# Kernel tuning notes

Measured on AMD Instinct MI355X. Metric: run time of the kernel, lower is better.

## Reference

```python
import jax, jax.numpy as jnp
import numpy as np

LN_EPS = 1e-5

def _layernorm(x, g, b):
    m = jnp.mean(x, axis=-1, keepdims=True)
    v = jnp.var(x, axis=-1, keepdims=True)
    return (x - m) * jax.lax.rsqrt(v + LN_EPS) * g + b

def setup_inputs() -> dict:
    key = jax.random.key(0)
    ks = jax.random.split(key, 8)
    H = 1024
    B, S = 8, 2048
    def xavier(k, fan_in, fan_out):
        lim = float(np.sqrt(6.0 / (fan_in + fan_out)))
        return jax.random.uniform(k, (fan_in, fan_out), jnp.float32, -lim, lim)
    return {
        "x": jax.random.normal(ks[0], (B, S, H), jnp.float32),
        "hidden_state": jnp.zeros((B, H), jnp.float32),
        "W_in": xavier(ks[1], H, 3 * H), "b_in": jnp.zeros((3 * H,), jnp.float32),
        "W_rec": xavier(ks[2], H, H), "b_rec": jnp.zeros((H,), jnp.float32),
        "W_gate": xavier(ks[3], H, 2 * H), "b_gate": jnp.zeros((2 * H,), jnp.float32),
        "W_out": xavier(ks[4], H, H), "b_out": jnp.zeros((H,), jnp.float32),
        "ln_g": jnp.ones((H,), jnp.float32), "ln_b": jnp.zeros((H,), jnp.float32),
    }

def reference(x, hidden_state, W_in, b_in, W_rec, b_rec, W_gate, b_gate, W_out, b_out, ln_g, ln_b):
    # x: [B, S, H]
    H = x.shape[-1]
    feats = jnp.einsum('bsh,hk->bsk', x, W_in) + b_in        # [B,S,3H]
    u, v, w = jnp.split(feats, 3, axis=-1)
    u = jax.nn.silu(u)
    v = jax.nn.silu(v)
    # scan over time: xs laid out [S, B, H]
    uvw = (u.swapaxes(0, 1), v.swapaxes(0, 1), w.swapaxes(0, 1))

    def step(h, xs_t):
        u_t, v_t, w_t = xs_t
        gf = h @ W_gate + b_gate                              # [B,2H]
        gv, gt = jnp.split(gf, 2, axis=-1)
        gate = jax.nn.sigmoid(gv) * jax.nn.silu(gt)
        rec = h @ W_rec + b_rec
        nh = gate * rec + (1.0 - gate) * (u_t * v_t + w_t)
        nh = _layernorm(nh, ln_g, ln_b)                       # dropout inactive (eval)
        return nh, nh

    final_hidden, hiddens = jax.lax.scan(step, hidden_state, uvw)  # hiddens: [S,B,H]
    output = jnp.einsum('sbh,hk->bsk', hiddens, W_out) + b_out     # [B,S,H]
    return output, final_hidden
```

## Files before the change

### kernel.cpp

```cpp
#include <hip/hip_runtime.h>
#include <stdint.h>
#include <stddef.h>

typedef _Float16 f16;
typedef __attribute__((ext_vector_type(8))) _Float16 f16x8;
typedef __attribute__((ext_vector_type(4))) _Float16 f16x4;
typedef __attribute__((ext_vector_type(4))) float     f32x4;
typedef unsigned long long u64;

#define NB 8
#define NS 2048
#define NHID 1024
#define NWG 64

__device__ __forceinline__ float fsig(float x)  { return 1.f/(1.f+__expf(-x)); }
__device__ __forceinline__ float fsilu(float x) { return x/(1.f+__expf(-x)); }

__global__ __launch_bounds__(256) void k_cvt_f16(const float* __restrict__ in,
                                                 f16* __restrict__ out, int n) {
  int i = (blockIdx.x*blockDim.x + threadIdx.x)*4;
  int stride = gridDim.x*blockDim.x*4;
  for (; i < n; i += stride) {
    f32x4 v = *(const f32x4*)(in + i);
    f16x4 o = { (f16)v[0], (f16)v[1], (f16)v[2], (f16)v[3] };
    *(f16x4*)(out + i) = o;
  }
}

__global__ __launch_bounds__(256) void k_transpose_cvt(const float* __restrict__ W,
                                                       f16* __restrict__ Wt,
                                                       int K, int N) {
  __shared__ float tile[32][33];
  int k0 = blockIdx.x*32, n0 = blockIdx.y*32;
  int tx = threadIdx.x & 31, ty = threadIdx.x >> 5;
  for (int i = ty; i < 32; i += 8) tile[i][tx] = W[(size_t)(k0+i)*N + n0 + tx];
  __syncthreads();
  for (int i = ty; i < 32; i += 8) Wt[(size_t)(n0+i)*K + k0 + tx] = (f16)tile[tx][i];
}

__global__ __launch_bounds__(256) void k_gemm1(const f16* __restrict__ A,
                                               const f16* __restrict__ Bt,
                                               const float* __restrict__ b_in,
                                               f16* __restrict__ z) {
  __shared__ f16 As[2][128*64];
  __shared__ f16 Bs[2][3][32*64];
  const int tid  = threadIdx.x;
  const int row0 = blockIdx.x * 128;
  const int j0   = blockIdx.y * 32;
  const int lane = tid & 63, wave = tid >> 6;
  const int wm = wave >> 1, wj = wave & 1;

  f32x4 acc[4][3];
  const f32x4 zv = {0.f,0.f,0.f,0.f};
#pragma unroll
  for (int m = 0; m < 4; ++m)
#pragma unroll
    for (int s = 0; s < 3; ++s) acc[m][s] = zv;

  f16x8 ar[4]; f16x8 br[3];

  auto loadT = [&](int kt) {
    int k0 = kt*64;
#pragma unroll
    for (int i = 0; i < 4; ++i) {
      int c = tid + i*256; int r = c >> 3;
      ar[i] = *(const f16x8*)(A + (size_t)(row0 + r)*1024 + k0 + (c & 7)*8);
    }
#pragma unroll
    for (int i = 0; i < 3; ++i) {
      int c = tid + i*256; int strip = c >> 8; int cc = c & 255; int r = cc >> 3;
      br[i] = *(const f16x8*)(Bt + (size_t)(strip*1024 + j0 + r)*1024 + k0 + (cc & 7)*8);
    }
  };
  auto writeT = [&](int buf) {
#pragma unroll
    for (int i = 0; i < 4; ++i) {
      int c = tid + i*256; int r = c >> 3; int kb = (c & 7)*16;
      *(f16x8*)((char*)As[buf] + r*128 + (kb ^ ((r & 7) << 4))) = ar[i];
    }
#pragma unroll
    for (int i = 0; i < 3; ++i) {
      int c = tid + i*256; int strip = c >> 8; int cc = c & 255; int r = cc >> 3; int kb = (cc & 7)*16;
      *(f16x8*)((char*)Bs[buf][strip] + r*128 + (kb ^ ((r & 7) << 4))) = br[i];
    }
  };
  auto compute = [&](int buf) {
    const char* Ab = (const char*)As[buf];
#pragma unroll
    for (int kk = 0; kk < 2; ++kk) {
      int kq = kk*64 + ((lane >> 4) << 4);
      f16x8 af[4];
#pragma unroll
      for (int mt = 0; mt < 4; ++mt) {
        int r = wm*64 + mt*16 + (lane & 15);
        af[mt] = *(const f16x8*)(Ab + r*128 + (kq ^ ((r & 7) << 4)));
      }
#pragma unroll
      for (int st = 0; st < 3; ++st) {
        int cB = wj*16 + (lane & 15);
        f16x8 bf = *(const f16x8*)((const char*)Bs[buf][st] + cB*128 + (kq ^ ((cB & 7) << 4)));
#pragma unroll
        for (int mt = 0; mt < 4; ++mt)
          acc[mt][st] = __builtin_amdgcn_mfma_f32_16x16x32_f16(af[mt], bf, acc[mt][st], 0, 0, 0);
      }
    }
  };

  loadT(0); writeT(0);
  __syncthreads();
  for (int kt = 0; kt < 16; ++kt) {
    int cur = kt & 1;
    if (kt + 1 < 16) loadT(kt+1);
    compute(cur);
    if (kt + 1 < 16) writeT(cur ^ 1);
    __syncthreads();
  }

  const int jc = j0 + wj*16 + (lane & 15);
  const float bu = b_in[jc], bv = b_in[1024 + jc], bw = b_in[2048 + jc];
#pragma unroll
  for (int mt = 0; mt < 4; ++mt) {
#pragma unroll
    for (int i = 0; i < 4; ++i) {
      int r = row0 + wm*64 + mt*16 + ((lane >> 4) << 2) + i;
      float u = acc[mt][0][i] + bu;
      float v = acc[mt][1][i] + bv;
      float w = acc[mt][2][i] + bw;
      float zz = fsilu(u)*fsilu(v) + w;
      int b_ = r >> 11, s_ = r & 2047;
      z[(((size_t)s_*64 + (jc >> 4))*8 + b_)*16 + (jc & 15)] = (f16)zz;
    }
  }
}

__global__ __launch_bounds__(256) void k_gemm3(const f16* __restrict__ A,
                                               const f16* __restrict__ Bt,
                                               const float* __restrict__ b_out,
                                               float* __restrict__ out) {
  __shared__ f16 As[2][128*64];
  __shared__ f16 Bs[2][32*64];
  const int tid  = threadIdx.x;
  const int row0 = blockIdx.x * 128;
  const int n0   = blockIdx.y * 32;
  const int lane = tid & 63, wave = tid >> 6;
  const int wm = wave >> 1, wn = wave & 1;

  f32x4 acc[4];
  const f32x4 zv = {0.f,0.f,0.f,0.f};
#pragma unroll
  for (int m = 0; m < 4; ++m) acc[m] = zv;

  f16x8 ar[4]; f16x8 br1;

  auto loadT = [&](int kt) {
    int k0 = kt*64;
#pragma unroll
    for (int i = 0; i < 4; ++i) {
      int c = tid + i*256; int r = c >> 3;
      ar[i] = *(const f16x8*)(A + (size_t)(row0 + r)*1024 + k0 + (c & 7)*8);
    }
    { int c = tid; int r = c >> 3;
      br1 = *(const f16x8*)(Bt + (size_t)(n0 + r)*1024 + k0 + (c & 7)*8); }
  };
  auto writeT = [&](int buf) {
#pragma unroll
    for (int i = 0; i < 4; ++i) {
      int c = tid + i*256; int r = c >> 3; int kb = (c & 7)*16;
      *(f16x8*)((char*)As[buf] + r*128 + (kb ^ ((r & 7) << 4))) = ar[i];
    }
    { int c = tid; int r = c >> 3; int kb = (c & 7)*16;
      *(f16x8*)((char*)Bs[buf] + r*128 + (kb ^ ((r & 7) << 4))) = br1; }
  };
  auto compute = [&](int buf) {
    const char* Ab = (const char*)As[buf];
#pragma unroll
    for (int kk = 0; kk < 2; ++kk) {
      int kq = kk*64 + ((lane >> 4) << 4);
      int cB = wn*16 + (lane & 15);
      f16x8 bf = *(const f16x8*)((const char*)Bs[buf] + cB*128 + (kq ^ ((cB & 7) << 4)));
#pragma unroll
      for (int mt = 0; mt < 4; ++mt) {
        int r = wm*64 + mt*16 + (lane & 15);
        f16x8 af = *(const f16x8*)(Ab + r*128 + (kq ^ ((r & 7) << 4)));
        acc[mt] = __builtin_amdgcn_mfma_f32_16x16x32_f16(af, bf, acc[mt], 0, 0, 0);
      }
    }
  };

  loadT(0); writeT(0);
  __syncthreads();
  for (int kt = 0; kt < 16; ++kt) {
    int cur = kt & 1;
    if (kt + 1 < 16) loadT(kt+1);
    compute(cur);
    if (kt + 1 < 16) writeT(cur ^ 1);
    __syncthreads();
  }

  const int n = n0 + wn*16 + (lane & 15);
  const float bo = b_out[n];
#pragma unroll
  for (int mt = 0; mt < 4; ++mt) {
#pragma unroll
    for (int i = 0; i < 4; ++i) {
      int r = row0 + wm*64 + mt*16 + ((lane >> 4) << 2) + i;
      int s = r >> 3, b = r & 7;
      out[(size_t)b*(NS*NHID) + (size_t)s*NHID + n] = acc[mt][i] + bo;
    }
  }
}

#define SCAN_LDS 70848
__global__ __launch_bounds__(256, 1) void k_scan(
    const float* __restrict__ h0g,  const float* __restrict__ Wg,
    const float* __restrict__ bg,   const float* __restrict__ Wr,
    const float* __restrict__ brv,  const float* __restrict__ lng_g,
    const float* __restrict__ lnb_g,const f16* __restrict__ z,
    f16* __restrict__ hid,          u64* __restrict__ hpub,
    float* __restrict__ finalh) {
  extern __shared__ char smem[];
  f16*   hlds = (f16*)smem;
  f16*   nhst = (f16*)(smem + 33536);
  float* red  = (float*)(smem + 49920);
  float* lng  = (float*)(smem + 62208);
  float* lnb  = (float*)(smem + 66304);
  float* bia  = (float*)(smem + 70400);
  f16*   pub  = (f16*)(smem + 70592);

  const int tid  = threadIdx.x;
  const int wg   = blockIdx.x;
  const int wave = tid >> 6, lane = tid & 63;
  const int r8   = tid >> 5, g32 = tid & 31;
  const int rr   = (tid >> 4) & 7, cc = tid & 15;

  f16x8 wf0[8], wf1[8], wf2[8];
  {
    const int cB = wg*16 + (lane & 15);
    const int kq = (lane >> 4) << 3;
#pragma unroll
    for (int ks = 0; ks < 8; ++ks) {
      int k = wave*256 + ks*32 + kq;
      f16x8 a, b, c;
#pragma unroll
      for (int e = 0; e < 8; ++e) {
        a[e] = (f16)Wg[(size_t)(k+e)*2048 + cB];
        b[e] = (f16)Wg[(size_t)(k+e)*2048 + 1024 + cB];
        c[e] = (f16)Wr[(size_t)(k+e)*1024 + cB];
      }
      wf0[ks] = a; wf1[ks] = b; wf2[ks] = c;
    }
  }
  for (int i = tid; i < 1024; i += 256) { lng[i] = lng_g[i]; lnb[i] = lnb_g[i]; }
  if (tid < 48)
    bia[tid] = (tid < 16) ? bg[wg*16 + tid]
             : (tid < 32) ? bg[1024 + wg*16 + (tid-16)]
                          : brv[wg*16 + (tid-32)];
  for (int i = tid; i < 8*1048; i += 256) hlds[8*1048 + i] = (f16)0.f;
  __syncthreads();

  for (int t = 0; t <= NS; ++t) {
    f16 zreg = (f16)0.f;
    if (t < NS && tid < 128) zreg = z[(((size_t)t*64 + wg)*8 + rr)*16 + cc];

    if (t == 0) {
#pragma unroll
      for (int j = 0; j < 8; ++j) {
        f32x4 v = *(const f32x4*)(h0g + r8*1024 + (j*32 + g32)*4);
        int colb = j*128 + g32*4;
        f16x4 hv = { (f16)v[0], (f16)v[1], (f16)v[2], (f16)v[3] };
        *(f16x4*)(hlds + r8*1048 + colb) = hv;
      }
      __syncthreads();
    } else {
      const u64* src = hpub + (size_t)(t & 1)*2816;
      u64 got[11];
      unsigned ok = 0;
      while (!ok) {
        ok = 1;
#pragma unroll
        for (int i = 0; i < 11; ++i) {
          got[i] = __hip_atomic_load(src + i*256 + tid,
                                     __ATOMIC_RELAXED, __HIP_MEMORY_SCOPE_AGENT);
          ok &= (unsigned)((unsigned)(got[i] >> 48) == (unsigned)t);
        }
      }
#pragma unroll
      for (int i = 0; i < 11; ++i) {
        int gidx = i*256 + tid;
        int wgI = gidx / 44;
        int slot = gidx - wgI*44;
        if (slot < 43) {
          int s0 = slot*3;
          u64 g = got[i];
#pragma unroll
          for (int e = 0; e < 3; ++e) {
            int s = s0 + e;
            if (s < 128) {
              unsigned short hb = (unsigned short)(g >> (16*e));
              nhst[((s >> 4))*1024 + wgI*16 + (s & 15)] = __builtin_bit_cast(f16, hb);
            }
          }
        }
      }
      __syncthreads();

      float sum = 0.f, sq = 0.f;
#pragma unroll
      for (int j = 0; j < 8; ++j) {
        f16x4 hv = *(const f16x4*)(nhst + r8*1024 + (j*32 + g32)*4);
#pragma unroll
        for (int e = 0; e < 4; ++e) { float v = (float)hv[e]; sum += v; sq += v*v; }
      }
#pragma unroll
      for (int off = 16; off > 0; off >>= 1) {
        sum += __shfl_xor(sum, off, 32);
        sq  += __shfl_xor(sq,  off, 32);
      }
      float m  = sum * (1.f/1024.f);
      float va = sq  * (1.f/1024.f) - m*m;
      float rs = rsqrtf(va + 1e-5f);
#pragma unroll
      for (int j = 0; j < 8; ++j) {
        int colb = (j*32 + g32)*4;
        f16x4 hv = *(const f16x4*)(nhst + r8*1024 + colb);
        f16x4 o;
#pragma unroll
        for (int e = 0; e < 4; ++e)
          o[e] = (f16)(((float)hv[e] - m)*rs*lng[colb+e] + lnb[colb+e]);
        *(f16x4*)(hlds + r8*1048 + colb) = o;
      }
      __syncthreads();
    }

    if (t >= 1 && tid < 32) {
      int row = tid >> 2, ch = tid & 3;
      u64 v = *(const u64*)(hlds + row*1048 + wg*16 + ch*4);
      *(u64*)(hid + ((size_t)(t-1)*8 + row)*1024 + wg*16 + ch*4) = v;
    }
    if (t == NS) {
      if (tid < 128) finalh[rr*1024 + wg*16 + cc] = (float)hlds[rr*1048 + wg*16 + cc];
      break;
    }

    f32x4 acc0 = {0,0,0,0}, acc1 = {0,0,0,0}, acc2 = {0,0,0,0};
    {
      const char* hb = (const char*)hlds + (lane & 15)*2096;
      const int kbyte0 = (wave*256 + ((lane >> 4) << 3))*2;
#pragma unroll
      for (int ks = 0; ks < 8; ++ks) {
        f16x8 af = *(const f16x8*)(hb + kbyte0 + ks*64);
        acc0 = __builtin_amdgcn_mfma_f32_16x16x32_f16(af, wf0[ks], acc0, 0, 0, 0);
        acc1 = __builtin_amdgcn_mfma_f32_16x16x32_f16(af, wf1[ks], acc1, 0, 0, 0);
        acc2 = __builtin_amdgcn_mfma_f32_16x16x32_f16(af, wf2[ks], acc2, 0, 0, 0);
      }
    }
    *(f32x4*)(red + ((wave*3 + 0)*64 + lane)*4) = acc0;
    *(f32x4*)(red + ((wave*3 + 1)*64 + lane)*4) = acc1;
    *(f32x4*)(red + ((wave*3 + 2)*64 + lane)*4) = acc2;
    __syncthreads();

    if (tid < 128) {
      int li  = ((rr >> 2) << 4) + cc;
      int reg = rr & 3;
      float s0 = 0.f, s1 = 0.f, s2 = 0.f;
#pragma unroll
      for (int q = 0; q < 4; ++q) {
        s0 += red[((q*3 + 0)*64 + li)*4 + reg];
        s1 += red[((q*3 + 1)*64 + li)*4 + reg];
        s2 += red[((q*3 + 2)*64 + li)*4 + reg];
      }
      float gv = s0 + bia[cc];
      float gt = s1 + bia[16 + cc];
      float rc = s2 + bia[32 + cc];
      float gate = fsig(gv) * fsilu(gt);
      float nh   = gate*rc + (1.f - gate)*(float)zreg;
      pub[rr*16 + cc] = (f16)nh;
    }
    __syncthreads();

    if (tid < 44) {
      int s0 = tid*3;
      unsigned short b0 = (s0     < 128) ? __builtin_bit_cast(unsigned short, pub[s0])     : (unsigned short)0;
      unsigned short b1 = (s0 + 1 < 128) ? __builtin_bit_cast(unsigned short, pub[s0 + 1]) : (unsigned short)0;
      unsigned short b2 = (s0 + 2 < 128) ? __builtin_bit_cast(unsigned short, pub[s0 + 2]) : (unsigned short)0;
      u64 v = (u64)b0 | ((u64)b1 << 16) | ((u64)b2 << 32) | ((u64)(unsigned)(t + 1) << 48);
      __hip_atomic_store(hpub + (size_t)((t + 1) & 1)*2816 + wg*44 + tid, v,
                         __ATOMIC_RELAXED, __HIP_MEMORY_SCOPE_AGENT);
    }
  }
}

extern "C" void kernel_launch(void* const* d_in, const int* in_sizes, int n_in,
                              void* d_out, int out_size, void* d_ws, size_t ws_size,
                              hipStream_t stream) {
  const float* x      = (const float*)d_in[0];
  const float* h0     = (const float*)d_in[1];
  const float* W_in   = (const float*)d_in[2];
  const float* b_in   = (const float*)d_in[3];
  const float* W_rec  = (const float*)d_in[4];
  const float* b_rec  = (const float*)d_in[5];
  const float* W_gate = (const float*)d_in[6];
  const float* b_gate = (const float*)d_in[7];
  const float* W_out  = (const float*)d_in[8];
  const float* b_out  = (const float*)d_in[9];
  const float* ln_g   = (const float*)d_in[10];
  const float* ln_b   = (const float*)d_in[11];
  float* out = (float*)d_out;

  char* ws = (char*)d_ws;
  f16*   x_f16  = (f16*)(ws);
  f16*   Wt_in  = (f16*)(ws + 33554432);
  f16*   Wt_out = (f16*)(ws + 39845888);
  f16*   z      = (f16*)(ws + 41943040);
  f16*   hid    = (f16*)(ws + 75497472);
  u64*   hpub   = (u64*)(ws + 109051904);

  k_cvt_f16<<<2048, 256, 0, stream>>>(x, x_f16, NB*NS*NHID);
  { dim3 g(32, 96); k_transpose_cvt<<<g, 256, 0, stream>>>(W_in,  Wt_in,  1024, 3072); }
  { dim3 g(32, 32); k_transpose_cvt<<<g, 256, 0, stream>>>(W_out, Wt_out, 1024, 1024); }

  { dim3 g(128, 32); k_gemm1<<<g, 256, 0, stream>>>(x_f16, Wt_in, b_in, z); }

  hipFuncSetAttribute((const void*)k_scan, hipFuncAttributeMaxDynamicSharedMemorySize, SCAN_LDS);
  k_scan<<<NWG, 256, SCAN_LDS, stream>>>(h0, W_gate, b_gate, W_rec, b_rec,
                                         ln_g, ln_b, z, hid, hpub,
                                         out + (size_t)NB*NS*NHID);

  { dim3 g(128, 32); k_gemm3<<<g, 256, 0, stream>>>(hid, Wt_out, b_out, out); }
}
```

Baseline: 8.517 ms.

## Repack hidden-state publish format to two halves per word and fuse layernorm into unpack

Changes the cross-workgroup publication of the new hidden state from 3 halves plus a 16-bit tag per 64-bit word to 2 halves plus a 32-bit step tag, written directly by the computing threads. This removes the staging LDS buffer and one barrier on the producer side. On the consumer side, the polled values are kept in registers and the layernorm statistics are reduced with shuffles and a small LDS step, with no scatter into an LDS staging array. The cost is more polled words per step (4096 instead of 2816) and more register pressure from holding 32 values.

Measured after the change: 7.113 ms. 16.5% less time.

```diff
diff --git a/kernel.cpp b/kernel.cpp
--- a/kernel.cpp
+++ b/kernel.cpp
@@ -6,6 +6,7 @@
 typedef __attribute__((ext_vector_type(8))) _Float16 f16x8;
 typedef __attribute__((ext_vector_type(4))) _Float16 f16x4;
 typedef __attribute__((ext_vector_type(4))) float     f32x4;
+typedef __attribute__((ext_vector_type(2))) float     f32x2;
 typedef unsigned long long u64;
 
 #define NB 8
@@ -210,7 +211,7 @@
   }
 }
 
-#define SCAN_LDS 70848
+#define SCAN_LDS 54208
 __global__ __launch_bounds__(256, 1) void k_scan(
     const float* __restrict__ h0g,  const float* __restrict__ Wg,
     const float* __restrict__ bg,   const float* __restrict__ Wr,
@@ -220,18 +221,17 @@
     float* __restrict__ finalh) {
   extern __shared__ char smem[];
   f16*   hlds = (f16*)smem;
-  f16*   nhst = (f16*)(smem + 33536);
-  float* red  = (float*)(smem + 49920);
-  float* lng  = (float*)(smem + 62208);
-  float* lnb  = (float*)(smem + 66304);
-  float* bia  = (float*)(smem + 70400);
-  f16*   pub  = (f16*)(smem + 70592);
+  float* redw = (float*)(smem + 33536);
+  f32x2* gb   = (f32x2*)(smem + 45824);
+  float* bia  = (float*)(smem + 54016);
 
   const int tid  = threadIdx.x;
   const int wg   = blockIdx.x;
   const int wave = tid >> 6, lane = tid & 63;
   const int r8   = tid >> 5, g32 = tid & 31;
   const int rr   = (tid >> 4) & 7, cc = tid & 15;
+  const int rL   = tid & 7;
+  const int c2L  = (tid & 63) >> 3;
 
   f16x8 wf0[8], wf1[8], wf2[8];
   {
@@ -250,7 +250,7 @@
       wf0[ks] = a; wf1[ks] = b; wf2[ks] = c;
     }
   }
-  for (int i = tid; i < 1024; i += 256) { lng[i] = lng_g[i]; lnb[i] = lnb_g[i]; }
+  for (int i = tid; i < 1024; i += 256) { f32x2 p = { lng_g[i], lnb_g[i] }; gb[i] = p; }
   if (tid < 48)
     bia[tid] = (tid < 16) ? bg[wg*16 + tid]
              : (tid < 32) ? bg[1024 + wg*16 + (tid-16)]
@@ -272,62 +272,54 @@
       }
       __syncthreads();
     } else {
-      const u64* src = hpub + (size_t)(t & 1)*2816;
-      u64 got[11];
-      unsigned ok = 0;
-      while (!ok) {
-        ok = 1;
-#pragma unroll
-        for (int i = 0; i < 11; ++i) {
+      const u64* src = hpub + (size_t)(t & 1)*4096;
+      u64 got[16];
+      for (;;) {
+        unsigned ok = 1;
+#pragma unroll
+        for (int i = 0; i < 16; ++i) {
           got[i] = __hip_atomic_load(src + i*256 + tid,
                                      __ATOMIC_RELAXED, __HIP_MEMORY_SCOPE_AGENT);
-          ok &= (unsigned)((unsigned)(got[i] >> 48) == (unsigned)t);
+          ok &= (unsigned)((unsigned)(got[i] >> 32) == (unsigned)t);
         }
-      }
-#pragma unroll
-      for (int i = 0; i < 11; ++i) {
-        int gidx = i*256 + tid;
-        int wgI = gidx / 44;
-        int slot = gidx - wgI*44;
-        if (slot < 43) {
-          int s0 = slot*3;
-          u64 g = got[i];
-#pragma unroll
-          for (int e = 0; e < 3; ++e) {
-            int s = s0 + e;
-            if (s < 128) {
-              unsigned short hb = (unsigned short)(g >> (16*e));
-              nhst[((s >> 4))*1024 + wgI*16 + (s & 15)] = __builtin_bit_cast(f16, hb);
-            }
-          }
-        }
-      }
+        if (ok) break;
+      }
+      float vals[32];
+      float sum = 0.f, sq = 0.f;
+#pragma unroll
+      for (int i = 0; i < 16; ++i) {
+        unsigned lo = (unsigned)got[i];
+        float va = (float)__builtin_bit_cast(f16, (unsigned short)(lo & 0xffff));
+        float vb = (float)__builtin_bit_cast(f16, (unsigned short)(lo >> 16));
+        vals[2*i] = va; vals[2*i+1] = vb;
+        sum += va + vb; sq += va*va + vb*vb;
+      }
+#pragma unroll
+      for (int off = 8; off <= 32; off <<= 1) {
+        sum += __shfl_xor(sum, off, 64);
+        sq  += __shfl_xor(sq,  off, 64);
+      }
+      if (lane < 8) { f32x2 p = { sum, sq }; ((f32x2*)redw)[wave*8 + lane] = p; }
       __syncthreads();
-
-      float sum = 0.f, sq = 0.f;
-#pragma unroll
-      for (int j = 0; j < 8; ++j) {
-        f16x4 hv = *(const f16x4*)(nhst + r8*1024 + (j*32 + g32)*4);
-#pragma unroll
-        for (int e = 0; e < 4; ++e) { float v = (float)hv[e]; sum += v; sq += v*v; }
-      }
-#pragma unroll
-      for (int off = 16; off > 0; off >>= 1) {
-        sum += __shfl_xor(sum, off, 32);
-        sq  += __shfl_xor(sq,  off, 32);
-      }
-      float m  = sum * (1.f/1024.f);
-      float va = sq  * (1.f/1024.f) - m*m;
+      float s4 = 0.f, q4 = 0.f;
+#pragma unroll
+      for (int w2 = 0; w2 < 4; ++w2) {
+        f32x2 p = ((const f32x2*)redw)[w2*8 + rL];
+        s4 += p[0]; q4 += p[1];
+      }
+      float m  = s4 * (1.f/1024.f);
+      float va = q4 * (1.f/1024.f) - m*m;
       float rs = rsqrtf(va + 1e-5f);
 #pragma unroll
-      for (int j = 0; j < 8; ++j) {
-        int colb = (j*32 + g32)*4;
-        f16x4 hv = *(const f16x4*)(nhst + r8*1024 + colb);
-        f16x4 o;
-#pragma unroll
-        for (int e = 0; e < 4; ++e)
-          o[e] = (f16)(((float)hv[e] - m)*rs*lng[colb+e] + lnb[colb+e]);
-        *(f16x4*)(hlds + r8*1048 + colb) = o;
+      for (int i = 0; i < 16; ++i) {
+        int wgI = i*4 + wave;
+        int col = wgI*16 + c2L*2;
+        f32x4 gg = *(const f32x4*)(gb + col);
+        float h0n = (vals[2*i]   - m)*rs*gg[0] + gg[1];
+        float h1n = (vals[2*i+1] - m)*rs*gg[2] + gg[3];
+        unsigned w32 = (unsigned)__builtin_bit_cast(unsigned short, (f16)h0n)
+                     | ((unsigned)__builtin_bit_cast(unsigned short, (f16)h1n) << 16);
+        *(unsigned*)((char*)hlds + rL*2096 + col*2) = w32;
       }
       __syncthreads();
     }
@@ -354,9 +346,9 @@
         acc2 = __builtin_amdgcn_mfma_f32_16x16x32_f16(af, wf2[ks], acc2, 0, 0, 0);
       }
     }
-    *(f32x4*)(red + ((wave*3 + 0)*64 + lane)*4) = acc0;
-    *(f32x4*)(red + ((wave*3 + 1)*64 + lane)*4) = acc1;
-    *(f32x4*)(red + ((wave*3 + 2)*64 + lane)*4) = acc2;
+    *(f32x4*)(redw + ((wave*3 + 0)*64 + lane)*4) = acc0;
+    *(f32x4*)(redw + ((wave*3 + 1)*64 + lane)*4) = acc1;
+    *(f32x4*)(redw + ((wave*3 + 2)*64 + lane)*4) = acc2;
     __syncthreads();
 
     if (tid < 128) {
@@ -365,27 +357,23 @@
       float s0 = 0.f, s1 = 0.f, s2 = 0.f;
 #pragma unroll
       for (int q = 0; q < 4; ++q) {
-        s0 += red[((q*3 + 0)*64 + li)*4 + reg];
-        s1 += red[((q*3 + 1)*64 + li)*4 + reg];
-        s2 += red[((q*3 + 2)*64 + li)*4 + reg];
+        s0 += redw[((q*3 + 0)*64 + li)*4 + reg];
+        s1 += redw[((q*3 + 1)*64 + li)*4 + reg];
+        s2 += redw[((q*3 + 2)*64 + li)*4 + reg];
       }
       float gv = s0 + bia[cc];
       float gt = s1 + bia[16 + cc];
       float rc = s2 + bia[32 + cc];
       float gate = fsig(gv) * fsilu(gt);
       float nh   = gate*rc + (1.f - gate)*(float)zreg;
-      pub[rr*16 + cc] = (f16)nh;
-    }
-    __syncthreads();
-
-    if (tid < 44) {
-      int s0 = tid*3;
-      unsigned short b0 = (s0     < 128) ? __builtin_bit_cast(unsigned short, pub[s0])     : (unsigned short)0;
-      unsigned short b1 = (s0 + 1 < 128) ? __builtin_bit_cast(unsigned short, pub[s0 + 1]) : (unsigned short)0;
-      unsigned short b2 = (s0 + 2 < 128) ? __builtin_bit_cast(unsigned short, pub[s0 + 2]) : (unsigned short)0;
-      u64 v = (u64)b0 | ((u64)b1 << 16) | ((u64)b2 << 32) | ((u64)(unsigned)(t + 1) << 48);
-      __hip_atomic_store(hpub + (size_t)((t + 1) & 1)*2816 + wg*44 + tid, v,
-                         __ATOMIC_RELAXED, __HIP_MEMORY_SCOPE_AGENT);
+      float nh_hi = __shfl_xor(nh, 1, 64);
+      if ((cc & 1) == 0) {
+        u64 v = (u64)__builtin_bit_cast(unsigned short, (f16)nh)
+              | ((u64)__builtin_bit_cast(unsigned short, (f16)nh_hi) << 16)
+              | ((u64)(unsigned)(t + 1) << 32);
+        __hip_atomic_store(hpub + (size_t)((t + 1) & 1)*4096 + wg*64 + (cc >> 1)*8 + rr,
+                           v, __ATOMIC_RELAXED, __HIP_MEMORY_SCOPE_AGENT);
+      }
     }
   }
 }
```
